# Kernel optimization log

Measured on AMD Instinct MI355X. Metric: run time of the kernel, lower is better.

## Reference

```python
import jax, jax.numpy as jnp
import numpy as np

N_NODES = 50000

def _sage_conv(x, src, dst, W_l, b_l, W_r):
    # mean-aggregate neighbor features: messages x[src] summed into dst
    msgs = x[src]                                   # [E, d]
    agg = jax.ops.segment_sum(msgs, dst, num_segments=N_NODES)  # [N, d]
    ones = jnp.ones((src.shape[0],), dtype=x.dtype)
    cnt = jax.ops.segment_sum(ones, dst, num_segments=N_NODES)  # [N]
    agg = agg / jnp.maximum(cnt, 1.0)[:, None]
    return agg @ W_l + b_l + x @ W_r


def setup_inputs() -> dict:
    key = jax.random.key(0)
    ks = jax.random.split(key, 8)
    d_in, hid, out = 64, 128, 64
    x = jax.random.normal(ks[0], (N_NODES, d_in), dtype=jnp.float32)
    edge_index = jax.random.randint(ks[1], (2, 1600000), 0, N_NODES, dtype=jnp.int64)
    def w(k, a, b):
        return jax.random.normal(k, (a, b), dtype=jnp.float32) / np.sqrt(a)
    return {
        "x": x,
        "edge_index": edge_index,
        "W_l1": w(ks[2], d_in, hid), "b_l1": jnp.zeros((hid,), jnp.float32),
        "W_r1": w(ks[3], d_in, hid),
        "W_l2": w(ks[4], hid, hid), "b_l2": jnp.zeros((hid,), jnp.float32),
        "W_r2": w(ks[5], hid, hid),
        "W_out": w(ks[6], hid, out), "b_out": jnp.zeros((out,), jnp.float32),
    }


def reference(x, edge_index, W_l1, b_l1, W_r1, W_l2, b_l2, W_r2, W_out, b_out):
    src, dst = edge_index[0], edge_index[1]
    h = jax.nn.relu(_sage_conv(x, src, dst, W_l1, b_l1, W_r1))
    h = jax.nn.relu(_sage_conv(h, src, dst, W_l2, b_l2, W_r2))
    return h @ W_out + b_out
```

## Files before the change

kernel.cpp:

```cpp
#include <hip/hip_runtime.h>


typedef unsigned short ushort_t;
typedef unsigned int uint_t;
typedef unsigned char uchar_t;
typedef __attribute__((ext_vector_type(8))) short short8;
typedef __attribute__((ext_vector_type(8))) ushort_t ushort8;
typedef __attribute__((ext_vector_type(4))) float f32x4;

#define BKT_SHIFT 7
#define BKT_NODES 128
#define BKT_CAP   5120
#define EPB       4096
#define QSCALE    32.0f
#define QINV      0.03125f
#define XQSCALE   16.0f

__device__ inline ushort_t bf16_rne(float v) {
    uint_t u = __float_as_uint(v);
    u += 0x7fffu + ((u >> 16) & 1u);
    return (ushort_t)(u >> 16);
}
__device__ inline float bf16_to_f(ushort_t h) {
    return __uint_as_float((uint_t)h << 16);
}


struct WPack {
    const float* srcp[5];
    ushort_t* dstp[5];
    int K[5], N[5], beg[5], end[5];
};

__global__ __launch_bounds__(1024)
void k_work(const int* __restrict__ src, const int* __restrict__ dst,
            uint_t* __restrict__ pairs, int* __restrict__ bcnt, int E, int nbk,
            int bbl, const float* __restrict__ x, ushort_t* __restrict__ xh,
            ushort_t* __restrict__ xl, uchar_t* __restrict__ xq,
            int NS, WPack wp, int total) {
    int tid = threadIdx.x;
    if (blockIdx.x >= bbl) {
        int t = (blockIdx.x - bbl) * 1024 + tid;
        if (t < NS) {
            float v = x[t];
            ushort_t h = bf16_rne(v);
            xh[t] = h;
            xl[t] = bf16_rne(v - bf16_to_f(h));
            int qv = (int)(v * XQSCALE + 128.5f);
            qv = qv < 0 ? 0 : (qv > 255 ? 255 : qv);
            xq[t] = (uchar_t)qv;
            return;
        }
        t -= NS;
        if (t >= total) return;
#pragma unroll
        for (int m = 0; m < 5; ++m) {
            if (t >= wp.beg[m] && t < wp.end[m]) {
                int i = t - wp.beg[m];
                int K = wp.K[m], N = wp.N[m];
                int k = i / N, nn = i % N;
                int NT = N >> 4;
                int kt = k >> 5, bq = (k >> 3) & 3, j = k & 7;
                int nt = nn >> 4, lane = (bq << 4) | (nn & 15);
                int base = (((kt * NT + nt) << 6) + lane) * 8 + j;
                int halfsz = (K >> 5) * NT * 512;
                float v = wp.srcp[m][i];
                ushort_t h = bf16_rne(v);
                wp.dstp[m][base] = h;
                wp.dstp[m][halfsz + base] = bf16_rne(v - bf16_to_f(h));
            }
        }
        return;
    }

    __shared__ int h[4][512];
    int sub = tid & 3;
    for (int i = tid; i < 4 * 512; i += 1024) ((int*)h)[i] = 0;
    __syncthreads();

    int e = blockIdx.x * EPB + tid * 4;
    bool full = (e + 4 <= E);
    int4 d4 = {0, 0, 0, 0}, s4 = {0, 0, 0, 0};
    if (full) {
        d4 = *(const int4*)(dst + e);
        s4 = *(const int4*)(src + e);
        atomicAdd(&h[sub][d4.x >> BKT_SHIFT], 1);
        atomicAdd(&h[sub][d4.y >> BKT_SHIFT], 1);
        atomicAdd(&h[sub][d4.z >> BKT_SHIFT], 1);
        atomicAdd(&h[sub][d4.w >> BKT_SHIFT], 1);
    } else {
        for (int t = e; t < E && t < e + 4; ++t)
            atomicAdd(&h[sub][dst[t] >> BKT_SHIFT], 1);
    }
    __syncthreads();
    for (int i = tid; i < nbk; i += 1024) {
        int c0 = h[0][i], c1 = h[1][i], c2 = h[2][i], c3 = h[3][i];
        int c = c0 + c1 + c2 + c3;
        int bs = c ? atomicAdd(&bcnt[i], c) : 0;
        h[0][i] = bs; h[1][i] = bs + c0; h[2][i] = bs + c0 + c1;
        h[3][i] = bs + c0 + c1 + c2;
    }
    __syncthreads();
    if (full) {
        int dd[4] = {d4.x, d4.y, d4.z, d4.w};
        int ss[4] = {s4.x, s4.y, s4.z, s4.w};
#pragma unroll
        for (int t = 0; t < 4; ++t) {
            int b = dd[t] >> BKT_SHIFT;
            int r = atomicAdd(&h[sub][b], 1);
            pairs[(size_t)b * BKT_CAP + r] =
                (uint_t)(ss[t] & 0xFFFF) | ((uint_t)(dd[t] & (BKT_NODES - 1)) << 16);
        }
    } else {
        for (int t = e; t < E && t < e + 4; ++t) {
            int d = dst[t];
            int b = d >> BKT_SHIFT;
            int r = atomicAdd(&h[sub][b], 1);
            pairs[(size_t)b * BKT_CAP + r] =
                (uint_t)(src[t] & 0xFFFF) | ((uint_t)(d & (BKT_NODES - 1)) << 16);
        }
    }
}


__global__ __launch_bounds__(1024) void k_csr(const uint_t* __restrict__ pairs,
                                              const int* __restrict__ bcnt,
                                              int* __restrict__ off,
                                              ushort_t* __restrict__ col, int n) {
    __shared__ int hist[BKT_NODES];
    __shared__ int s[BKT_NODES];
    __shared__ int cur[BKT_NODES];
    __shared__ int bofs_s;
    int b = blockIdx.x, tid = threadIdx.x;
    if (tid < 64) {
        int p = 0;
        for (int i = tid; i < b; i += 64) p += bcnt[i];
#pragma unroll
        for (int m = 1; m < 64; m <<= 1) p += __shfl_xor(p, m);
        if (tid == 0) bofs_s = p;
    }
    if (tid < BKT_NODES) hist[tid] = 0;
    __syncthreads();
    int bofs = bofs_s;
    int cnt = bcnt[b];
    const uint_t* p = pairs + (size_t)b * BKT_CAP;
    for (int i = tid; i < cnt; i += 1024) atomicAdd(&hist[(p[i] >> 16) & 127], 1);
    __syncthreads();
    int v = (tid < BKT_NODES) ? hist[tid] : 0;
    if (tid < BKT_NODES) s[tid] = v;
    __syncthreads();
    for (int ofs = 1; ofs < BKT_NODES; ofs <<= 1) {
        int t = (tid >= ofs && tid < BKT_NODES) ? s[tid - ofs] : 0;
        __syncthreads();
        if (tid < BKT_NODES) s[tid] += t;
        __syncthreads();
    }
    if (tid < BKT_NODES) {
        int excl = bofs + s[tid] - v;
        int node = b * BKT_NODES + tid;
        if (node <= n) off[node] = excl;
        cur[tid] = excl;
    }
    __syncthreads();
    for (int i = tid; i < cnt; i += 1024) {
        uint_t pk = p[i];
        int pos = atomicAdd(&cur[(pk >> 16) & 127], 1);
        col[pos] = (ushort_t)(pk & 0xFFFF);
    }
}

__device__ inline void unpack2(uint_t v, uint_t& a, uint_t& b) {
    a = (v & 0xFFu) | ((v << 8) & 0x00FF0000u);
    b = ((v >> 16) & 0xFFu) | ((v >> 8) & 0x00FF0000u);
}

__device__ inline f32x4 mfma3(f32x4 acc, short8 ah, short8 al, short8 bh, short8 bl) {
    acc = __builtin_amdgcn_mfma_f32_16x16x32_bf16(ah, bh, acc, 0, 0, 0);
    acc = __builtin_amdgcn_mfma_f32_16x16x32_bf16(al, bh, acc, 0, 0, 0);
    acc = __builtin_amdgcn_mfma_f32_16x16x32_bf16(ah, bl, acc, 0, 0, 0);
    return acc;
}


__global__ __launch_bounds__(512)
void k_layer1(const uchar_t* __restrict__ xq, const ushort_t* __restrict__ xh,
              const ushort_t* __restrict__ xl,
              const int* __restrict__ off, const ushort_t* __restrict__ col,
              const ushort_t* __restrict__ Wlp, const ushort_t* __restrict__ Wrp,
              const float* __restrict__ bias, ushort_t* __restrict__ Oh,
              uchar_t* __restrict__ Oq, int n) {
    __shared__ ushort_t Ahs[64][72];
    __shared__ ushort_t Als[64][72];
    int tid = threadIdx.x, waveid = tid >> 6, lane = tid & 63;
    int base = blockIdx.x * 64;
    int grp = lane >> 3, li = lane & 7;
    int nl = waveid * 8 + grp;
    int node = base + nl;
    int nd = node < n ? node : n - 1;
    int s0 = off[nd], s1 = off[nd + 1], last = s1 - 1;
    uint_t ae0 = 0, ao0 = 0, ae1 = 0, ao1 = 0;
    const uchar_t* fb = xq + li * 8;
    for (int e = s0; e < s1; e += 8) {
        int c[8];
#pragma unroll
        for (int j = 0; j < 8; ++j) c[j] = col[min(e + j, last)];
        uint2 q[8];
#pragma unroll
        for (int j = 0; j < 8; ++j) q[j] = *(const uint2*)(fb + (size_t)c[j] * 64);
#pragma unroll
        for (int j = 0; j < 8; ++j) {
            uint_t m = (e + j <= last) ? 0xFFFFFFFFu : 0u;
            uint_t a, b;
            unpack2(q[j].x & m, a, b); ae0 += a; ao0 += b;
            unpack2(q[j].y & m, a, b); ae1 += a; ao1 += b;
        }
    }
    {
        int deg = s1 - s0;
        float inv = 1.f / (XQSCALE * fmaxf((float)deg, 1.f));
        float c8 = deg > 0 ? 8.f : 0.f;
        uint_t f[8] = {ae0 & 0xFFFFu, ae0 >> 16, ao0 & 0xFFFFu, ao0 >> 16,
                       ae1 & 0xFFFFu, ae1 >> 16, ao1 & 0xFFFFu, ao1 >> 16};
        ushort_t vh[8], vl[8];
#pragma unroll
        for (int k = 0; k < 8; ++k) {
            float v = (float)f[k] * inv - c8;
            ushort_t h = bf16_rne(v);
            vh[k] = h;
            vl[k] = bf16_rne(v - bf16_to_f(h));
        }
        *(ushort8*)&Ahs[nl][li * 8] = *(ushort8*)vh;
        *(ushort8*)&Als[nl][li * 8] = *(ushort8*)vl;
    }
    __syncthreads();

    int rowt = waveid >> 1, c0w = waveid & 1;
    int colq = lane & 15, quad = lane >> 4;
    int arow = rowt * 16 + colq;
    short8 fah[2], fal[2], fxh[2], fxl[2];
#pragma unroll
    for (int kt = 0; kt < 2; ++kt) {
        fah[kt] = *(const short8*)&Ahs[arow][kt * 32 + quad * 8];
        fal[kt] = *(const short8*)&Als[arow][kt * 32 + quad * 8];
    }
    int grow = base + arow; if (grow >= n) grow = n - 1;
#pragma unroll
    for (int kt = 0; kt < 2; ++kt) {
        fxh[kt] = *(const short8*)(xh + (size_t)grow * 64 + kt * 32 + quad * 8);
        fxl[kt] = *(const short8*)(xl + (size_t)grow * 64 + kt * 32 + quad * 8);
    }
#pragma unroll
    for (int t = 0; t < 4; ++t) {
        int nt = t * 2 + c0w;
        float bv = bias[nt * 16 + colq];
        f32x4 acc = (f32x4){bv, bv, bv, bv};
#pragma unroll
        for (int kt = 0; kt < 2; ++kt) {
            const ushort_t* pL = Wlp + ((size_t)((kt * 8 + nt) << 6) + lane) * 8;
            acc = mfma3(acc, fah[kt], fal[kt],
                        *(const short8*)pL, *(const short8*)(pL + 8192));
            const ushort_t* pR = Wrp + ((size_t)((kt * 8 + nt) << 6) + lane) * 8;
            acc = mfma3(acc, fxh[kt], fxl[kt],
                        *(const short8*)pR, *(const short8*)(pR + 8192));
        }
        int rowb = base + rowt * 16 + quad * 4;
        int cix = nt * 16 + colq;
#pragma unroll
        for (int r = 0; r < 4; ++r) {
            int row = rowb + r;
            if (row < n) {
                float v = fmaxf(acc[r], 0.f);
                Oh[(size_t)row * 128 + cix] = bf16_rne(v);
                int qv = (int)(v * QSCALE + 0.5f);
                Oq[(size_t)row * 128 + cix] = (uchar_t)(qv > 255 ? 255 : qv);
            }
        }
    }
}


__global__ __launch_bounds__(512)
void k_layer2(const uchar_t* __restrict__ h1q, const int* __restrict__ off,
              const ushort_t* __restrict__ col, const ushort_t* __restrict__ h1h,
              const ushort_t* __restrict__ Wlp, const ushort_t* __restrict__ Wrp,
              const float* __restrict__ b2, const ushort_t* __restrict__ Wop,
              const float* __restrict__ bo, float* __restrict__ out, int n) {
    __shared__ ushort_t Ah[64][136];
    __shared__ ushort_t Al[64][136];
    int tid = threadIdx.x, waveid = tid >> 6, lane = tid & 63;
    int base = blockIdx.x * 64;
    int grp = lane >> 3, li = lane & 7;
    int nl = waveid * 8 + grp;
    int node = base + nl;
    int nd = node < n ? node : n - 1;
    int s0 = off[nd], s1 = off[nd + 1], last = s1 - 1;
    uint_t ae[4] = {0, 0, 0, 0}, ao[4] = {0, 0, 0, 0};
    const uchar_t* fb = h1q + li * 16;
    for (int e = s0; e < s1; e += 8) {
        int c[8];
#pragma unroll
        for (int j = 0; j < 8; ++j) c[j] = col[min(e + j, last)];
        uint4 q[8];
#pragma unroll
        for (int j = 0; j < 8; ++j) q[j] = *(const uint4*)(fb + (size_t)c[j] * 128);
#pragma unroll
        for (int j = 0; j < 8; ++j) {
            uint_t m = (e + j <= last) ? 0xFFFFFFFFu : 0u;
            const uint_t* u = (const uint_t*)&q[j];
#pragma unroll
            for (int k = 0; k < 4; ++k) {
                uint_t a, b;
                unpack2(u[k] & m, a, b);
                ae[k] += a;
                ao[k] += b;
            }
        }
    }
    {
        float inv = QINV / fmaxf((float)(s1 - s0), 1.f);
        ushort_t vh[16], vl[16];
#pragma unroll
        for (int k = 0; k < 4; ++k) {
            uint_t f[4] = {ae[k] & 0xFFFFu, ae[k] >> 16,
                           ao[k] & 0xFFFFu, ao[k] >> 16};
#pragma unroll
            for (int b = 0; b < 4; ++b) {
                float v = (float)f[b] * inv;
                ushort_t h = bf16_rne(v);
                vh[k * 4 + b] = h;
                vl[k * 4 + b] = bf16_rne(v - bf16_to_f(h));
            }
        }
        *(ushort8*)&Ah[nl][li * 16] = *(ushort8*)&vh[0];
        *(ushort8*)&Ah[nl][li * 16 + 8] = *(ushort8*)&vh[8];
        *(ushort8*)&Al[nl][li * 16] = *(ushort8*)&vl[0];
        *(ushort8*)&Al[nl][li * 16 + 8] = *(ushort8*)&vl[8];
    }
    __syncthreads();

    int rowt = waveid >> 1, c0w = waveid & 1;
    int colx = lane & 15, quad = lane >> 4;
    int arow = rowt * 16 + colx;
    int grow = base + arow; if (grow >= n) grow = n - 1;
    short8 gah[4], gal[4], sh[4];
#pragma unroll
    for (int kt = 0; kt < 4; ++kt) {
        gah[kt] = *(const short8*)&Ah[arow][kt * 32 + quad * 8];
        gal[kt] = *(const short8*)&Al[arow][kt * 32 + quad * 8];
        sh[kt]  = *(const short8*)(h1h + (size_t)grow * 128 + kt * 32 + quad * 8);
    }
    __syncthreads();

    f32x4 accd[4];
#pragma unroll
    for (int t = 0; t < 4; ++t) {
        int nt = t * 2 + c0w;
        float bv = b2[nt * 16 + colx];
        f32x4 acc = (f32x4){bv, bv, bv, bv};
#pragma unroll
        for (int kt = 0; kt < 4; ++kt) {
            const ushort_t* pL = Wlp + ((size_t)((kt * 8 + nt) << 6) + lane) * 8;
            acc = mfma3(acc, gah[kt], gal[kt],
                        *(const short8*)pL, *(const short8*)(pL + 16384));
            const ushort_t* pR = Wrp + ((size_t)((kt * 8 + nt) << 6) + lane) * 8;
            short8 bh = *(const short8*)pR;
            short8 bl = *(const short8*)(pR + 16384);
            acc = __builtin_amdgcn_mfma_f32_16x16x32_bf16(sh[kt], bh, acc, 0, 0, 0);
            acc = __builtin_amdgcn_mfma_f32_16x16x32_bf16(sh[kt], bl, acc, 0, 0, 0);
        }
        accd[t] = acc;
    }
#pragma unroll
    for (int t = 0; t < 4; ++t) {
        int nt = t * 2 + c0w;
#pragma unroll
        for (int r = 0; r < 4; ++r) {
            int row = rowt * 16 + quad * 4 + r;
            float v = fmaxf(accd[t][r], 0.f);
            ushort_t h = bf16_rne(v);
            Ah[row][nt * 16 + colx] = h;
            Al[row][nt * 16 + colx] = bf16_rne(v - bf16_to_f(h));
        }
    }
    __syncthreads();

    int rowt2 = waveid >> 1;
    int arow2 = rowt2 * 16 + colx;
    short8 hh[4], hl[4];
#pragma unroll
    for (int kt = 0; kt < 4; ++kt) {
        hh[kt] = *(const short8*)&Ah[arow2][kt * 32 + quad * 8];
        hl[kt] = *(const short8*)&Al[arow2][kt * 32 + quad * 8];
    }
#pragma unroll
    for (int t2 = 0; t2 < 2; ++t2) {
        int nt2 = t2 * 2 + (waveid & 1);
        float bv = bo[nt2 * 16 + colx];
        f32x4 acc2 = (f32x4){bv, bv, bv, bv};
#pragma unroll
        for (int kt = 0; kt < 4; ++kt) {
            const ushort_t* p = Wop + ((size_t)((kt * 4 + nt2) << 6) + lane) * 8;
            acc2 = mfma3(acc2, hh[kt], hl[kt],
                         *(const short8*)p, *(const short8*)(p + 8192));
        }
#pragma unroll
        for (int r = 0; r < 4; ++r) {
            int row = base + rowt2 * 16 + quad * 4 + r;
            if (row < n) out[(size_t)row * 64 + nt2 * 16 + colx] = acc2[r];
        }
    }
}


static inline size_t align256(size_t x) { return (x + 255) & ~(size_t)255; }

extern "C" void kernel_launch(void* const* d_in, const int* in_sizes, int n_in,
                              void* d_out, int out_size, void* d_ws, size_t ws_size,
                              hipStream_t stream) {
    const float* x   = (const float*)d_in[0];
    const int*   ei  = (const int*)d_in[1];
    const float* Wl1 = (const float*)d_in[2];
    const float* bl1 = (const float*)d_in[3];
    const float* Wr1 = (const float*)d_in[4];
    const float* Wl2 = (const float*)d_in[5];
    const float* bl2 = (const float*)d_in[6];
    const float* Wr2 = (const float*)d_in[7];
    const float* Wo  = (const float*)d_in[8];
    const float* bo  = (const float*)d_in[9];

    const int N = in_sizes[0] / 64;
    const int E = in_sizes[1] / 2;
    const int* src = ei;
    const int* dst = ei + E;
    const int nbk = (N + BKT_NODES - 1) >> BKT_SHIFT;

    char* ws = (char*)d_ws;
    int* off = (int*)ws;            ws += align256((size_t)(N + 1) * 4);
    int* bcnt = (int*)ws;           ws += align256((size_t)nbk * 4);
    uint_t* pairs = (uint_t*)ws;    ws += align256((size_t)nbk * BKT_CAP * 4);
    ushort_t* col = (ushort_t*)ws;  ws += align256((size_t)E * 2);
    ushort_t* xh  = (ushort_t*)ws;  ws += align256((size_t)N * 64 * 2);
    ushort_t* xl  = (ushort_t*)ws;  ws += align256((size_t)N * 64 * 2);
    uchar_t*  xq  = (uchar_t*)ws;   ws += align256((size_t)N * 64);
    ushort_t* h1h = (ushort_t*)ws;  ws += align256((size_t)N * 128 * 2);
    uchar_t*  h1q = (uchar_t*)ws;   ws += align256((size_t)N * 128);
    ushort_t* Wl1p = (ushort_t*)ws; ws += align256((size_t)2 * 64 * 128 * 2);
    ushort_t* Wr1p = (ushort_t*)ws; ws += align256((size_t)2 * 64 * 128 * 2);
    ushort_t* Wl2p = (ushort_t*)ws; ws += align256((size_t)2 * 128 * 128 * 2);
    ushort_t* Wr2p = (ushort_t*)ws; ws += align256((size_t)2 * 128 * 128 * 2);
    ushort_t* Wop  = (ushort_t*)ws; ws += align256((size_t)2 * 128 * 64 * 2);

    WPack wp;
    wp.srcp[0] = Wl1; wp.dstp[0] = Wl1p; wp.K[0] = 64;  wp.N[0] = 128;
    wp.srcp[1] = Wr1; wp.dstp[1] = Wr1p; wp.K[1] = 64;  wp.N[1] = 128;
    wp.srcp[2] = Wl2; wp.dstp[2] = Wl2p; wp.K[2] = 128; wp.N[2] = 128;
    wp.srcp[3] = Wr2; wp.dstp[3] = Wr2p; wp.K[3] = 128; wp.N[3] = 128;
    wp.srcp[4] = Wo;  wp.dstp[4] = Wop;  wp.K[4] = 128; wp.N[4] = 64;
    int acc_el = 0;
    for (int m = 0; m < 5; ++m) {
        wp.beg[m] = acc_el; acc_el += wp.K[m] * wp.N[m]; wp.end[m] = acc_el;
    }
    int NS = N * 64;

    hipMemsetAsync(bcnt, 0, (size_t)nbk * 4, stream);
    int bbl = (E + EPB - 1) / EPB;
    int pbl = (NS + acc_el + 1023) / 1024;
    k_work<<<bbl + pbl, 1024, 0, stream>>>(src, dst, pairs, bcnt, E, nbk, bbl,
                                           x, xh, xl, xq, NS, wp, acc_el);

    k_csr<<<nbk, 1024, 0, stream>>>(pairs, bcnt, off, col, N);

    k_layer1<<<(N + 63) / 64, 512, 0, stream>>>(xq, xh, xl, off, col, Wl1p,
                                                Wr1p, bl1, h1h, h1q, N);

    k_layer2<<<(N + 63) / 64, 512, 0, stream>>>(h1q, off, col, h1h, Wl2p,
                                                Wr2p, bl2, Wop, bo,
                                                (float*)d_out, N);
}
```

Measured before the change: 213.9 us.

## Shrink GNN layer blocks to 256 threads and widen layer-1 gathers

Both layer kernels now run with 256 threads per block and a higher occupancy hint. Layer 1 uses 4 lanes per node with 16-byte gathers instead of 8 lanes with 8-byte gathers, and each wave computes all 8 output column tiles. Layer 2 processes 32 nodes per block instead of 64. The byte unpacking now uses two mask operations in place of the old shift-and-merge, with the element order permuted to match. The aim is more resident waves to hide gather latency and fewer ALU ops per edge, at the cost of more MFMA work per wave in layer 1 and more, smaller blocks in layer 2.

```diff
diff --git a/kernel.cpp b/kernel.cpp
--- a/kernel.cpp
+++ b/kernel.cpp
@@ -169,11 +169,6 @@
     }
 }
 
-__device__ inline void unpack2(uint_t v, uint_t& a, uint_t& b) {
-    a = (v & 0xFFu) | ((v << 8) & 0x00FF0000u);
-    b = ((v >> 16) & 0xFFu) | ((v >> 8) & 0x00FF0000u);
-}
-
 __device__ inline f32x4 mfma3(f32x4 acc, short8 ah, short8 al, short8 bh, short8 bl) {
     acc = __builtin_amdgcn_mfma_f32_16x16x32_bf16(ah, bh, acc, 0, 0, 0);
     acc = __builtin_amdgcn_mfma_f32_16x16x32_bf16(al, bh, acc, 0, 0, 0);
@@ -182,7 +177,7 @@
 }
 
 
-__global__ __launch_bounds__(512)
+__global__ __launch_bounds__(256, 8)
 void k_layer1(const uchar_t* __restrict__ xq, const ushort_t* __restrict__ xh,
               const ushort_t* __restrict__ xl,
               const int* __restrict__ off, const ushort_t* __restrict__ col,
@@ -193,48 +188,57 @@
     __shared__ ushort_t Als[64][72];
     int tid = threadIdx.x, waveid = tid >> 6, lane = tid & 63;
     int base = blockIdx.x * 64;
-    int grp = lane >> 3, li = lane & 7;
-    int nl = waveid * 8 + grp;
+    int grp = lane >> 2, li = lane & 3;
+    int nl = waveid * 16 + grp;
     int node = base + nl;
     int nd = node < n ? node : n - 1;
     int s0 = off[nd], s1 = off[nd + 1], last = s1 - 1;
-    uint_t ae0 = 0, ao0 = 0, ae1 = 0, ao1 = 0;
-    const uchar_t* fb = xq + li * 8;
-    for (int e = s0; e < s1; e += 8) {
-        int c[8];
-#pragma unroll
-        for (int j = 0; j < 8; ++j) c[j] = col[min(e + j, last)];
-        uint2 q[8];
-#pragma unroll
-        for (int j = 0; j < 8; ++j) q[j] = *(const uint2*)(fb + (size_t)c[j] * 64);
-#pragma unroll
-        for (int j = 0; j < 8; ++j) {
+    uint_t ae[4] = {0, 0, 0, 0}, ao[4] = {0, 0, 0, 0};
+    const uchar_t* fb = xq + li * 16;
+    for (int e = s0; e < s1; e += 4) {
+        int c[4];
+#pragma unroll
+        for (int j = 0; j < 4; ++j) c[j] = col[min(e + j, last)];
+        uint4 q[4];
+#pragma unroll
+        for (int j = 0; j < 4; ++j) q[j] = *(const uint4*)(fb + (size_t)c[j] * 64);
+#pragma unroll
+        for (int j = 0; j < 4; ++j) {
             uint_t m = (e + j <= last) ? 0xFFFFFFFFu : 0u;
-            uint_t a, b;
-            unpack2(q[j].x & m, a, b); ae0 += a; ao0 += b;
-            unpack2(q[j].y & m, a, b); ae1 += a; ao1 += b;
+            const uint_t* u = (const uint_t*)&q[j];
+#pragma unroll
+            for (int k = 0; k < 4; ++k) {
+                uint_t v = u[k] & m;
+                ae[k] += v & 0x00FF00FFu;
+                ao[k] += (v >> 8) & 0x00FF00FFu;
+            }
         }
     }
     {
         int deg = s1 - s0;
         float inv = 1.f / (XQSCALE * fmaxf((float)deg, 1.f));
         float c8 = deg > 0 ? 8.f : 0.f;
-        uint_t f[8] = {ae0 & 0xFFFFu, ae0 >> 16, ao0 & 0xFFFFu, ao0 >> 16,
-                       ae1 & 0xFFFFu, ae1 >> 16, ao1 & 0xFFFFu, ao1 >> 16};
-        ushort_t vh[8], vl[8];
-#pragma unroll
-        for (int k = 0; k < 8; ++k) {
-            float v = (float)f[k] * inv - c8;
-            ushort_t h = bf16_rne(v);
-            vh[k] = h;
-            vl[k] = bf16_rne(v - bf16_to_f(h));
-        }
-        *(ushort8*)&Ahs[nl][li * 8] = *(ushort8*)vh;
-        *(ushort8*)&Als[nl][li * 8] = *(ushort8*)vl;
-    }
-    __syncthreads();
-
-    int rowt = waveid >> 1, c0w = waveid & 1;
+        ushort_t vh[16], vl[16];
+#pragma unroll
+        for (int k = 0; k < 4; ++k) {
+            uint_t f[4] = {ae[k] & 0xFFFFu, ao[k] & 0xFFFFu,
+                           ae[k] >> 16, ao[k] >> 16};
+#pragma unroll
+            for (int b = 0; b < 4; ++b) {
+                float v = (float)f[b] * inv - c8;
+                ushort_t h = bf16_rne(v);
+                vh[k * 4 + b] = h;
+                vl[k * 4 + b] = bf16_rne(v - bf16_to_f(h));
+            }
+        }
+        *(ushort8*)&Ahs[nl][li * 16] = *(ushort8*)&vh[0];
+        *(ushort8*)&Ahs[nl][li * 16 + 8] = *(ushort8*)&vh[8];
+        *(ushort8*)&Als[nl][li * 16] = *(ushort8*)&vl[0];
+        *(ushort8*)&Als[nl][li * 16 + 8] = *(ushort8*)&vl[8];
+    }
+    __syncthreads();
+
+    int rowt = waveid;
     int colq = lane & 15, quad = lane >> 4;
     int arow = rowt * 16 + colq;
     short8 fah[2], fal[2], fxh[2], fxl[2];
@@ -250,8 +254,7 @@
         fxl[kt] = *(const short8*)(xl + (size_t)grow * 64 + kt * 32 + quad * 8);
     }
 #pragma unroll
-    for (int t = 0; t < 4; ++t) {
-        int nt = t * 2 + c0w;
+    for (int nt = 0; nt < 8; ++nt) {
         float bv = bias[nt * 16 + colq];
         f32x4 acc = (f32x4){bv, bv, bv, bv};
 #pragma unroll
@@ -279,16 +282,16 @@
 }
 
 
-__global__ __launch_bounds__(512)
+__global__ __launch_bounds__(256, 8)
 void k_layer2(const uchar_t* __restrict__ h1q, const int* __restrict__ off,
               const ushort_t* __restrict__ col, const ushort_t* __restrict__ h1h,
               const ushort_t* __restrict__ Wlp, const ushort_t* __restrict__ Wrp,
               const float* __restrict__ b2, const ushort_t* __restrict__ Wop,
               const float* __restrict__ bo, float* __restrict__ out, int n) {
-    __shared__ ushort_t Ah[64][136];
-    __shared__ ushort_t Al[64][136];
+    __shared__ ushort_t Ah[32][136];
+    __shared__ ushort_t Al[32][136];
     int tid = threadIdx.x, waveid = tid >> 6, lane = tid & 63;
-    int base = blockIdx.x * 64;
+    int base = blockIdx.x * 32;
     int grp = lane >> 3, li = lane & 7;
     int nl = waveid * 8 + grp;
     int node = base + nl;
@@ -309,10 +312,9 @@
             const uint_t* u = (const uint_t*)&q[j];
 #pragma unroll
             for (int k = 0; k < 4; ++k) {
-                uint_t a, b;
-                unpack2(u[k] & m, a, b);
-                ae[k] += a;
-                ao[k] += b;
+                uint_t v = u[k] & m;
+                ae[k] += v & 0x00FF00FFu;
+                ao[k] += (v >> 8) & 0x00FF00FFu;
             }
         }
     }
@@ -321,8 +323,8 @@
         ushort_t vh[16], vl[16];
 #pragma unroll
         for (int k = 0; k < 4; ++k) {
-            uint_t f[4] = {ae[k] & 0xFFFFu, ae[k] >> 16,
-                           ao[k] & 0xFFFFu, ao[k] >> 16};
+            uint_t f[4] = {ae[k] & 0xFFFFu, ao[k] & 0xFFFFu,
+                           ae[k] >> 16, ao[k] >> 16};
 #pragma unroll
             for (int b = 0; b < 4; ++b) {
                 float v = (float)f[b] * inv;
@@ -470,10 +472,10 @@
 
     k_csr<<<nbk, 1024, 0, stream>>>(pairs, bcnt, off, col, N);
 
-    k_layer1<<<(N + 63) / 64, 512, 0, stream>>>(xq, xh, xl, off, col, Wl1p,
+    k_layer1<<<(N + 63) / 64, 256, 0, stream>>>(xq, xh, xl, off, col, Wl1p,
                                                 Wr1p, bl1, h1h, h1q, N);
 
-    k_layer2<<<(N + 63) / 64, 512, 0, stream>>>(h1q, off, col, h1h, Wl2p,
+    k_layer2<<<(N + 31) / 32, 256, 0, stream>>>(h1q, off, col, h1h, Wl2p,
                                                 Wr2p, bl2, Wop, bo,
                                                 (float*)d_out, N);
 }
```

Measured after the change: 207.0 us. 1.03x faster.
